# Performance work log

Measured on AMD Instinct MI355X. Metric: run time of the kernel, lower is better.

The kernel has to match this reference:

```python
import jax, jax.numpy as jnp
import numpy as np

NEG_SLOPE = 0.2  # PyG GATConv default negative_slope


def setup_inputs() -> dict:
    key = jax.random.key(0)
    ks = jax.random.split(key, 10)
    N, E, IN, H, C = 50000, 800000, 256, 4, 128
    return {
        "x": jax.random.normal(ks[0], (N, IN), jnp.float32),
        "edge_index": jax.random.randint(ks[1], (2, E), 0, N, jnp.int64),
        "W": jax.random.normal(ks[2], (IN, H * C), jnp.float32) * (1.0 / np.sqrt(IN)),
        "att_src": jax.random.normal(ks[3], (H, C), jnp.float32) * 0.1,
        "att_dst": jax.random.normal(ks[4], (H, C), jnp.float32) * 0.1,
        "gat_bias": jax.random.normal(ks[5], (C,), jnp.float32) * 0.01,
        "w1": jax.random.normal(ks[6], (C, C), jnp.float32) * (1.0 / np.sqrt(C)),
        "b1": jax.random.normal(ks[7], (C,), jnp.float32) * 0.01,
        "w2": jax.random.normal(ks[8], (C, 1), jnp.float32) * (1.0 / np.sqrt(C)),
        "b2": jax.random.normal(ks[9], (1,), jnp.float32) * 0.01,
    }


def _gat_conv(x, edge_index, W, att_src, att_dst, gat_bias):
    # PyG GATConv with concat=False (mean over heads), add_self_loops=True,
    # dropout inactive (eval mode).
    N = x.shape[0]
    H, C = att_src.shape
    xl = (x @ W).reshape(N, H, C)                       # [N,H,C] projected nodes
    a_src = jnp.einsum("nhc,hc->nh", xl, att_src)       # [N,H]
    a_dst = jnp.einsum("nhc,hc->nh", xl, att_dst)       # [N,H]
    loops = jnp.arange(N, dtype=edge_index.dtype)
    src = jnp.concatenate([edge_index[0], loops])        # [E+N]
    dst = jnp.concatenate([edge_index[1], loops])        # [E+N]
    logits = jax.nn.leaky_relu(a_src[src] + a_dst[dst], NEG_SLOPE)  # [E+N,H]
    # segment softmax over incoming edges of each dst node
    m = jax.ops.segment_max(logits, dst, num_segments=N)            # [N,H]
    e = jnp.exp(logits - m[dst])
    denom = jax.ops.segment_sum(e, dst, num_segments=N)             # [N,H]
    alpha = e / denom[dst]                                           # [E+N,H]
    # weighted scatter-add aggregation
    out = jax.ops.segment_sum(alpha[:, :, None] * xl[src], dst, num_segments=N)  # [N,H,C]
    return out.mean(axis=1) + gat_bias                   # concat=False -> head mean


def reference(x, edge_index, W, att_src, att_dst, gat_bias, w1, b1, w2, b2):
    h = _gat_conv(x, edge_index, W, att_src, att_dst, gat_bias)
    h = jax.nn.relu(h)
    h = jax.nn.relu(h @ w1 + b1)
    return (h @ w2 + b2)[:, 0]
```

## Files before the change

### kernel.cpp

```cpp
#include <hip/hip_runtime.h>
#include <hip/hip_bf16.h>


#define LEAKY(x) ((x) > 0.0f ? (x) : 0.2f * (x))
#define CAP 64

typedef __attribute__((ext_vector_type(8))) short short8v;
typedef __attribute__((ext_vector_type(4))) float floatx4;
typedef __attribute__((ext_vector_type(2))) float f32x2;
typedef __attribute__((ext_vector_type(2))) unsigned int u32x2;

__device__ __forceinline__ unsigned f2b(float f) {
    unsigned u = __float_as_uint(f);
    return (u + 0x7fffu + ((u >> 16) & 1u)) >> 16;
}

__device__ __forceinline__ float rlf(float v, int i) {
    return __uint_as_float(
        __builtin_amdgcn_readlane(__float_as_uint(v), (unsigned)i));
}

__device__ __forceinline__ void load_lds16(const void* g, void* lds) {
    __builtin_amdgcn_global_load_lds(
        (const __attribute__((address_space(1))) void*)g,
        (__attribute__((address_space(3))) void*)lds, 16, 0, 0);
}

__global__ __launch_bounds__(256) void prep_small(
    const float* __restrict__ W, const float* __restrict__ att_src,
    const float* __restrict__ att_dst, const float* __restrict__ w1,
    int* __restrict__ cnt, float* __restrict__ watt,
    ushort* __restrict__ WT2, ushort* __restrict__ w1t, int N) {
    int pb = blockIdx.x;
    int t = threadIdx.x;
    if (pb < 196) {
        int i = pb * 256 + t;
        if (i < N) cnt[i] = 0;
    } else if (pb < 204) {
        int idx = (pb - 196) * 256 + t;
        int k = idx >> 3;
        int h8 = idx & 7;
        int h = h8 & 3;
        const float* att = (h8 < 4) ? att_src : att_dst;
        const float* wrow = W + (size_t)k * 512 + h * 128;
        const float* arow = att + h * 128;
        float s = 0.f;
#pragma unroll 4
        for (int c = 0; c < 128; ++c) s += wrow[c] * arow[c];
        watt[h8 * 256 + k] = s;
    } else if (pb < 716) {
        int idx = (pb - 204) * 256 + t;
        int c = idx & 127;
        int h = (idx >> 7) & 3;
        int k = idx >> 9;
        WT2[c * 1024 + h * 256 + k] = (ushort)f2b(W[(size_t)k * 512 + h * 128 + c]);
    } else {
        int idx = (pb - 716) * 256 + t;
        int c = idx & 127;
        int k = idx >> 7;
        w1t[c * 128 + k] = (ushort)f2b(w1[(size_t)k * 128 + c]);
    }
}

__global__ void fill_lite(const int* __restrict__ ei, int E, int N,
                          int* __restrict__ cnt, int* __restrict__ esrc) {
    int e = blockIdx.x * 256 + threadIdx.x;
    if (e >= E + N) return;
    int s, d;
    if (e < E) {
        s = ei[e];
        d = ei[E + e];
    } else {
        s = d = e - E;
    }
    if (d < 0 || d >= N || s < 0 || s >= N) return;
    int slot = atomicAdd(&cnt[d], 1);
    if (slot < CAP) esrc[d * CAP + slot] = s;
}

__global__ __launch_bounds__(256) void cast_score(
    const float* __restrict__ x, const float* __restrict__ watt,
    ushort* __restrict__ xb, float* __restrict__ asrc,
    float* __restrict__ adst, int N) {
    int w = threadIdx.x >> 6, l = threadIdx.x & 63;
    int n = blockIdx.x * 4 + w;
    if (n >= N) return;
    float4 xv = *(const float4*)(x + (size_t)n * 256 + l * 4);
    ushort4 ub;
    ub.x = (ushort)f2b(xv.x);
    ub.y = (ushort)f2b(xv.y);
    ub.z = (ushort)f2b(xv.z);
    ub.w = (ushort)f2b(xv.w);
    *(ushort4*)(xb + (size_t)n * 256 + l * 4) = ub;

    float acc[8];
#pragma unroll
    for (int h8 = 0; h8 < 8; ++h8) {
        float4 wv = *(const float4*)(watt + h8 * 256 + l * 4);
        acc[h8] = xv.x * wv.x + xv.y * wv.y + xv.z * wv.z + xv.w * wv.w;
    }
#pragma unroll
    for (int o = 32; o; o >>= 1)
#pragma unroll
        for (int h8 = 0; h8 < 8; ++h8) acc[h8] += __shfl_xor(acc[h8], o);
    if (l == 0) {
#pragma unroll
        for (int h = 0; h < 4; ++h) {
            asrc[n * 4 + h] = acc[h];
            adst[n * 4 + h] = acc[4 + h];
        }
    }
}

#define EDGE_PK(w0, w1, w2, w3, g)                                           \
    {                                                                        \
        f32x2 _e01 = {__uint_as_float((g).x << 16),                          \
                      __uint_as_float((g).x & 0xffff0000u)};                 \
        f32x2 _e23 = {__uint_as_float((g).y << 16),                          \
                      __uint_as_float((g).y & 0xffff0000u)};                 \
        f32x2 _w;                                                            \
        _w = (f32x2){(w0), (w0)};                                            \
        acc[0][0] += _w * _e01; acc[0][1] += _w * _e23;                      \
        _w = (f32x2){(w1), (w1)};                                            \
        acc[1][0] += _w * _e01; acc[1][1] += _w * _e23;                      \
        _w = (f32x2){(w2), (w2)};                                            \
        acc[2][0] += _w * _e01; acc[2][1] += _w * _e23;                      \
        _w = (f32x2){(w3), (w3)};                                            \
        acc[3][0] += _w * _e01; acc[3][1] += _w * _e23;                      \
    }

__global__ __launch_bounds__(256) void aggregate_x(
    const ushort* __restrict__ xb, const int* __restrict__ cnt,
    const int* __restrict__ esrc, const float* __restrict__ asrc,
    const float* __restrict__ adst, ushort* __restrict__ G, int N) {
    const int t = threadIdx.x;
    const int wv = t >> 6, l = t & 63;
    const int n = blockIdx.x * 4 + wv;
    if (n >= N) return;
    const int beg = n * CAP;
    const int deg = min(cnt[n], CAP);
    const uint loff = (uint)l * 4u;

    float4 ad = ((const float4*)adst)[n];
    int s_l = 0;
    float4 wl = {0.f, 0.f, 0.f, 0.f};
    if (l < deg) {
        s_l = esrc[beg + l];
        float4 as = ((const float4*)asrc)[s_l];
        wl.x = __expf(LEAKY(as.x + ad.x));
        wl.y = __expf(LEAKY(as.y + ad.y));
        wl.z = __expf(LEAKY(as.z + ad.z));
        wl.w = __expf(LEAKY(as.w + ad.w));
    }
    float dx = wl.x, dy = wl.y, dz = wl.z, dw = wl.w;
#pragma unroll
    for (int o = 32; o; o >>= 1) {
        dx += __shfl_xor(dx, o);
        dy += __shfl_xor(dy, o);
        dz += __shfl_xor(dz, o);
        dw += __shfl_xor(dw, o);
    }
    const float sc[4] = {0.25f / dx, 0.25f / dy, 0.25f / dz, 0.25f / dw};

    f32x2 acc[4][2];
#pragma unroll
    for (int h = 0; h < 4; ++h) {
        acc[h][0] = (f32x2){0.f, 0.f};
        acc[h][1] = (f32x2){0.f, 0.f};
    }

    int i = 0;
    const int deg8 = deg & ~7;
    for (; i < deg8; i += 8) {
        int ss[8];
#pragma unroll
        for (int j = 0; j < 8; ++j)
            ss[j] = __builtin_amdgcn_readlane(s_l, i + j);
        uint2 gg[8];
#pragma unroll
        for (int j = 0; j < 8; ++j)
            gg[j] = *(const uint2*)(xb + ((uint)ss[j] * 256u + loff));
#pragma unroll
        for (int j = 0; j < 8; ++j) {
            float w0 = rlf(wl.x, i + j), w1 = rlf(wl.y, i + j);
            float w2 = rlf(wl.z, i + j), w3 = rlf(wl.w, i + j);
            EDGE_PK(w0, w1, w2, w3, gg[j]);
        }
    }
    for (; i < deg; ++i) {
        int s0 = __builtin_amdgcn_readlane(s_l, i);
        uint2 g0 = *(const uint2*)(xb + ((uint)s0 * 256u + loff));
        float w00 = rlf(wl.x, i), w01 = rlf(wl.y, i);
        float w02 = rlf(wl.z, i), w03 = rlf(wl.w, i);
        EDGE_PK(w00, w01, w02, w03, g0);
    }

#pragma unroll
    for (int h = 0; h < 4; ++h) {
        u32x2 o;
        o.x = f2b(acc[h][0][0] * sc[h]) | (f2b(acc[h][0][1] * sc[h]) << 16);
        o.y = f2b(acc[h][1][0] * sc[h]) | (f2b(acc[h][1][1] * sc[h]) << 16);
        *(u32x2*)(G + (size_t)n * 1024 + h * 256 + l * 4) = o;
    }
}

__global__ __launch_bounds__(256) void tail_kernel(
    const ushort* __restrict__ Gb,
    const ushort* __restrict__ Wstk,
    const ushort* __restrict__ w1t,
    const float* __restrict__ gat_bias, const float* __restrict__ b1,
    const float* __restrict__ w2, const float* __restrict__ b2,
    float* __restrict__ out, int N) {
    __shared__ char smem[33 * 1024];
    char* AlsB = smem;
    char* BlsB = smem + 16 * 1024;
    char* ndh = smem;
    float* sums = (float*)(smem + 32 * 1024);

    const int t = threadIdx.x;
    const int w = t >> 6;
    const int l = t & 63;
    const int wr = w >> 1, wc = w & 1;
    const int row0 = blockIdx.x * 128;

    float gbr[4], b1r[4], w2r[4];
#pragma unroll
    for (int n = 0; n < 4; ++n) {
        int cg = wc * 64 + n * 16 + (l & 15);
        gbr[n] = gat_bias[cg];
        b1r[n] = b1[cg];
        w2r[n] = w2[cg];
    }

    floatx4 acc[4][4];
#pragma unroll
    for (int m = 0; m < 4; ++m)
#pragma unroll
        for (int n = 0; n < 4; ++n) acc[m][n] = {0.f, 0.f, 0.f, 0.f};

    const int lr = l >> 3;
    const int kbyt = ((l & 7) ^ lr) << 4;
    const char* Abase = (const char*)Gb;
    const char* Bbase = (const char*)Wstk;

    for (int ks = 0; ks < 16; ++ks) {
        const int k0b = ks * 128;
#pragma unroll
        for (int c = 0; c < 4; ++c) {
            int rowt = w * 32 + c * 8 + lr;
            int rA = row0 + rowt;
            if (rA >= N) rA = N - 1;
            load_lds16(Abase + (size_t)rA * 2048 + k0b + kbyt,
                       AlsB + (w * 4 + c) * 1024);
            load_lds16(Bbase + (size_t)rowt * 2048 + k0b + kbyt,
                       BlsB + (w * 4 + c) * 1024);
        }
        __syncthreads();

#pragma unroll
        for (int kk = 0; kk < 2; ++kk) {
            const int kb_g = kk * 64 + (l >> 4) * 16;
            const int swz = (l & 7) << 4;
            short8v a[4], b[4];
#pragma unroll
            for (int m = 0; m < 4; ++m) {
                int row = wr * 64 + m * 16 + (l & 15);
                a[m] = *(const short8v*)(AlsB + row * 128 + (kb_g ^ swz));
            }
#pragma unroll
            for (int n = 0; n < 4; ++n) {
                int row = wc * 64 + n * 16 + (l & 15);
                b[n] = *(const short8v*)(BlsB + row * 128 + (kb_g ^ swz));
            }
#pragma unroll
            for (int m = 0; m < 4; ++m)
#pragma unroll
                for (int n = 0; n < 4; ++n)
                    acc[m][n] = __builtin_amdgcn_mfma_f32_16x16x32_bf16(
                        a[m], b[n], acc[m][n], 0, 0, 0);
        }
        __syncthreads();
    }

#pragma unroll
    for (int m = 0; m < 4; ++m) {
#pragma unroll
        for (int reg = 0; reg < 4; ++reg) {
            int r = wr * 64 + m * 16 + ((l >> 4) << 2) + reg;
            int srow = (r & 7) << 4;
#pragma unroll
            for (int n = 0; n < 4; ++n) {
                int c = wc * 64 + n * 16 + (l & 15);
                float v = acc[m][n][reg] + gbr[n];
                v = v > 0.f ? v : 0.f;
                *(ushort*)(ndh + r * 256 + ((2 * c) ^ srow)) = (ushort)f2b(v);
            }
        }
    }
    __syncthreads();

    floatx4 acc2[4][4];
#pragma unroll
    for (int m = 0; m < 4; ++m)
#pragma unroll
        for (int n = 0; n < 4; ++n) acc2[m][n] = {0.f, 0.f, 0.f, 0.f};

    const char* w1base = (const char*)w1t;
#pragma unroll
    for (int kk = 0; kk < 4; ++kk) {
        const int kb = kk * 64 + (l >> 4) * 16;
        short8v a2[4], b2f[4];
#pragma unroll
        for (int m = 0; m < 4; ++m) {
            int r = wr * 64 + m * 16 + (l & 15);
            a2[m] = *(const short8v*)(ndh + r * 256 + (kb ^ ((r & 7) << 4)));
        }
#pragma unroll
        for (int n = 0; n < 4; ++n) {
            int r = wc * 64 + n * 16 + (l & 15);
            b2f[n] = *(const short8v*)(w1base + r * 256 + kb);
        }
#pragma unroll
        for (int m = 0; m < 4; ++m)
#pragma unroll
            for (int n = 0; n < 4; ++n)
                acc2[m][n] = __builtin_amdgcn_mfma_f32_16x16x32_bf16(
                    a2[m], b2f[n], acc2[m][n], 0, 0, 0);
    }

    float part[4][4];
#pragma unroll
    for (int m = 0; m < 4; ++m)
#pragma unroll
        for (int reg = 0; reg < 4; ++reg) {
            float s = 0.f;
#pragma unroll
            for (int n = 0; n < 4; ++n) {
                float y = acc2[m][n][reg] + b1r[n];
                y = y > 0.f ? y : 0.f;
                s += y * w2r[n];
            }
            part[m][reg] = s;
        }
#pragma unroll
    for (int o = 1; o < 16; o <<= 1)
#pragma unroll
        for (int m = 0; m < 4; ++m)
#pragma unroll
            for (int reg = 0; reg < 4; ++reg)
                part[m][reg] += __shfl_xor(part[m][reg], o);
    if ((l & 15) == 0) {
#pragma unroll
        for (int m = 0; m < 4; ++m)
#pragma unroll
            for (int reg = 0; reg < 4; ++reg) {
                int r = wr * 64 + m * 16 + ((l >> 4) << 2) + reg;
                sums[wc * 128 + r] = part[m][reg];
            }
    }
    __syncthreads();
    if (t < 128) {
        int rg = row0 + t;
        if (rg < N) out[rg] = sums[t] + sums[128 + t] + b2[0];
    }
}

extern "C" void kernel_launch(void* const* d_in, const int* in_sizes, int n_in,
                              void* d_out, int out_size, void* d_ws,
                              size_t ws_size, hipStream_t stream) {
    const float* x = (const float*)d_in[0];
    const int* ei = (const int*)d_in[1];
    const float* W = (const float*)d_in[2];
    const float* att_src = (const float*)d_in[3];
    const float* att_dst = (const float*)d_in[4];
    const float* gat_bias = (const float*)d_in[5];
    const float* w1 = (const float*)d_in[6];
    const float* b1 = (const float*)d_in[7];
    const float* w2 = (const float*)d_in[8];
    const float* b2 = (const float*)d_in[9];
    float* out = (float*)d_out;

    const int N = in_sizes[0] / 256;
    const int E = in_sizes[1] / 2;

    size_t o = 0;
    char* wsb = (char*)d_ws;
    auto alloc = [&](size_t nbytes) -> void* {
        void* p = wsb + o;
        o += (nbytes + 255) & ~(size_t)255;
        return p;
    };
    float* asrc = (float*)alloc((size_t)N * 4 * 4);
    float* adst = (float*)alloc((size_t)N * 4 * 4);
    int* cnt = (int*)alloc((size_t)N * 4);
    int* esrc = (int*)alloc((size_t)N * CAP * 4);
    ushort* xb = (ushort*)alloc((size_t)N * 256 * 2);
    ushort* G = (ushort*)alloc((size_t)N * 1024 * 2);
    ushort* WT2 = (ushort*)alloc((size_t)128 * 1024 * 2);
    ushort* w1t = (ushort*)alloc((size_t)128 * 128 * 2);
    float* watt = (float*)alloc((size_t)8 * 256 * 4);

    prep_small<<<780, 256, 0, stream>>>(W, att_src, att_dst, w1, cnt, watt,
                                        WT2, w1t, N);
    cast_score<<<(N + 3) / 4, 256, 0, stream>>>(x, watt, xb, asrc, adst, N);
    fill_lite<<<(E + N + 255) / 256, 256, 0, stream>>>(ei, E, N, cnt, esrc);
    aggregate_x<<<(N + 3) / 4, 256, 0, stream>>>(xb, cnt, esrc, asrc, adst, G,
                                                 N);
    tail_kernel<<<(N + 127) / 128, 256, 0, stream>>>(
        G, WT2, w1t, gat_bias, b1, w2, b2, out, N);
}
```

Measured before the change: 198.2 us.

## Split wave into half-waves gathering two edges per step with 16-byte loads

The aggregation kernel now has each half of a wavefront gather a different source row. Every lane loads 16 bytes (8 bf16 channels) instead of 8, so two edges are processed per step, and the two halves' partial sums are combined with a cross-half shuffle before the bf16 store. This halves the number of gather load instructions and loop iterations per edge, at the cost of twice the accumulator registers and an extra reduction. The fill kernel also handles two edges per thread with half the blocks, which reduces launch and thread overhead.

Result: slower. 280.2 us (+41.4%).

```diff
diff --git a/kernel.cpp b/kernel.cpp
--- a/kernel.cpp
+++ b/kernel.cpp
@@ -8,7 +8,6 @@
 typedef __attribute__((ext_vector_type(8))) short short8v;
 typedef __attribute__((ext_vector_type(4))) float floatx4;
 typedef __attribute__((ext_vector_type(2))) float f32x2;
-typedef __attribute__((ext_vector_type(2))) unsigned int u32x2;
 
 __device__ __forceinline__ unsigned f2b(float f) {
     unsigned u = __float_as_uint(f);
@@ -64,18 +63,22 @@
 
 __global__ void fill_lite(const int* __restrict__ ei, int E, int N,
                           int* __restrict__ cnt, int* __restrict__ esrc) {
-    int e = blockIdx.x * 256 + threadIdx.x;
-    if (e >= E + N) return;
-    int s, d;
-    if (e < E) {
-        s = ei[e];
-        d = ei[E + e];
-    } else {
-        s = d = e - E;
-    }
-    if (d < 0 || d >= N || s < 0 || s >= N) return;
-    int slot = atomicAdd(&cnt[d], 1);
-    if (slot < CAP) esrc[d * CAP + slot] = s;
+    int base = (blockIdx.x * 256 + threadIdx.x) * 2;
+#pragma unroll
+    for (int q = 0; q < 2; ++q) {
+        int e = base + q;
+        if (e >= E + N) return;
+        int s, d;
+        if (e < E) {
+            s = ei[e];
+            d = ei[E + e];
+        } else {
+            s = d = e - E;
+        }
+        if (d < 0 || d >= N || s < 0 || s >= N) continue;
+        int slot = atomicAdd(&cnt[d], 1);
+        if (slot < CAP) esrc[d * CAP + slot] = s;
+    }
 }
 
 __global__ __launch_bounds__(256) void cast_score(
@@ -112,21 +115,27 @@
     }
 }
 
-#define EDGE_PK(w0, w1, w2, w3, g)                                           \
+#define BL(u) __uint_as_float((u) << 16)
+#define BH(u) __uint_as_float((u) & 0xffff0000u)
+#define PAIR_FMA(w0, w1, w2, w3, g)                                          \
     {                                                                        \
-        f32x2 _e01 = {__uint_as_float((g).x << 16),                          \
-                      __uint_as_float((g).x & 0xffff0000u)};                 \
-        f32x2 _e23 = {__uint_as_float((g).y << 16),                          \
-                      __uint_as_float((g).y & 0xffff0000u)};                 \
-        f32x2 _w;                                                            \
-        _w = (f32x2){(w0), (w0)};                                            \
-        acc[0][0] += _w * _e01; acc[0][1] += _w * _e23;                      \
-        _w = (f32x2){(w1), (w1)};                                            \
-        acc[1][0] += _w * _e01; acc[1][1] += _w * _e23;                      \
-        _w = (f32x2){(w2), (w2)};                                            \
-        acc[2][0] += _w * _e01; acc[2][1] += _w * _e23;                      \
-        _w = (f32x2){(w3), (w3)};                                            \
-        acc[3][0] += _w * _e01; acc[3][1] += _w * _e23;                      \
+        f32x2 _e0 = {BL((g).x), BH((g).x)};                                  \
+        f32x2 _e1 = {BL((g).y), BH((g).y)};                                  \
+        f32x2 _e2 = {BL((g).z), BH((g).z)};                                  \
+        f32x2 _e3 = {BL((g).w), BH((g).w)};                                  \
+        f32x2 _W;                                                            \
+        _W = (f32x2){(w0), (w0)};                                            \
+        acc[0][0] += _W * _e0; acc[0][1] += _W * _e1;                        \
+        acc[0][2] += _W * _e2; acc[0][3] += _W * _e3;                        \
+        _W = (f32x2){(w1), (w1)};                                            \
+        acc[1][0] += _W * _e0; acc[1][1] += _W * _e1;                        \
+        acc[1][2] += _W * _e2; acc[1][3] += _W * _e3;                        \
+        _W = (f32x2){(w2), (w2)};                                            \
+        acc[2][0] += _W * _e0; acc[2][1] += _W * _e1;                        \
+        acc[2][2] += _W * _e2; acc[2][3] += _W * _e3;                        \
+        _W = (f32x2){(w3), (w3)};                                            \
+        acc[3][0] += _W * _e0; acc[3][1] += _W * _e1;                        \
+        acc[3][2] += _W * _e2; acc[3][3] += _W * _e3;                        \
     }
 
 __global__ __launch_bounds__(256) void aggregate_x(
@@ -139,7 +148,8 @@
     if (n >= N) return;
     const int beg = n * CAP;
     const int deg = min(cnt[n], CAP);
-    const uint loff = (uint)l * 4u;
+    const int hf = l >> 5;
+    const uint coff = (uint)(l & 31) * 8u;
 
     float4 ad = ((const float4*)adst)[n];
     int s_l = 0;
@@ -162,45 +172,70 @@
     }
     const float sc[4] = {0.25f / dx, 0.25f / dy, 0.25f / dz, 0.25f / dw};
 
-    f32x2 acc[4][2];
-#pragma unroll
-    for (int h = 0; h < 4; ++h) {
-        acc[h][0] = (f32x2){0.f, 0.f};
-        acc[h][1] = (f32x2){0.f, 0.f};
-    }
+    f32x2 acc[4][4];
+#pragma unroll
+    for (int h = 0; h < 4; ++h)
+#pragma unroll
+        for (int c = 0; c < 4; ++c) acc[h][c] = (f32x2){0.f, 0.f};
 
     int i = 0;
-    const int deg8 = deg & ~7;
-    for (; i < deg8; i += 8) {
-        int ss[8];
-#pragma unroll
-        for (int j = 0; j < 8; ++j)
-            ss[j] = __builtin_amdgcn_readlane(s_l, i + j);
-        uint2 gg[8];
-#pragma unroll
-        for (int j = 0; j < 8; ++j)
-            gg[j] = *(const uint2*)(xb + ((uint)ss[j] * 256u + loff));
-#pragma unroll
-        for (int j = 0; j < 8; ++j) {
-            float w0 = rlf(wl.x, i + j), w1 = rlf(wl.y, i + j);
-            float w2 = rlf(wl.z, i + j), w3 = rlf(wl.w, i + j);
-            EDGE_PK(w0, w1, w2, w3, gg[j]);
-        }
-    }
-    for (; i < deg; ++i) {
-        int s0 = __builtin_amdgcn_readlane(s_l, i);
-        uint2 g0 = *(const uint2*)(xb + ((uint)s0 * 256u + loff));
-        float w00 = rlf(wl.x, i), w01 = rlf(wl.y, i);
-        float w02 = rlf(wl.z, i), w03 = rlf(wl.w, i);
-        EDGE_PK(w00, w01, w02, w03, g0);
-    }
-
-#pragma unroll
-    for (int h = 0; h < 4; ++h) {
-        u32x2 o;
+    for (; i + 8 <= deg; i += 8) {
+        uint4 g[4];
+#pragma unroll
+        for (int p = 0; p < 4; ++p) {
+            int se = __builtin_amdgcn_readlane(s_l, i + 2 * p);
+            int so = __builtin_amdgcn_readlane(s_l, i + 2 * p + 1);
+            int su = hf ? so : se;
+            g[p] = *(const uint4*)(xb + ((uint)su * 256u + coff));
+        }
+#pragma unroll
+        for (int p = 0; p < 4; ++p) {
+            int ie = i + 2 * p, io = ie + 1;
+            float w0 = hf ? rlf(wl.x, io) : rlf(wl.x, ie);
+            float w1 = hf ? rlf(wl.y, io) : rlf(wl.y, ie);
+            float w2 = hf ? rlf(wl.z, io) : rlf(wl.z, ie);
+            float w3 = hf ? rlf(wl.w, io) : rlf(wl.w, ie);
+            PAIR_FMA(w0, w1, w2, w3, g[p]);
+        }
+    }
+    for (; i + 2 <= deg; i += 2) {
+        int se = __builtin_amdgcn_readlane(s_l, i);
+        int so = __builtin_amdgcn_readlane(s_l, i + 1);
+        int su = hf ? so : se;
+        uint4 g = *(const uint4*)(xb + ((uint)su * 256u + coff));
+        float w0 = hf ? rlf(wl.x, i + 1) : rlf(wl.x, i);
+        float w1 = hf ? rlf(wl.y, i + 1) : rlf(wl.y, i);
+        float w2 = hf ? rlf(wl.z, i + 1) : rlf(wl.z, i);
+        float w3 = hf ? rlf(wl.w, i + 1) : rlf(wl.w, i);
+        PAIR_FMA(w0, w1, w2, w3, g);
+    }
+    if (i < deg) {
+        int se = __builtin_amdgcn_readlane(s_l, i);
+        uint4 g = *(const uint4*)(xb + ((uint)se * 256u + coff));
+        float w0 = hf ? 0.f : rlf(wl.x, i);
+        float w1 = hf ? 0.f : rlf(wl.y, i);
+        float w2 = hf ? 0.f : rlf(wl.z, i);
+        float w3 = hf ? 0.f : rlf(wl.w, i);
+        PAIR_FMA(w0, w1, w2, w3, g);
+    }
+
+#pragma unroll
+    for (int h = 0; h < 4; ++h)
+#pragma unroll
+        for (int c = 0; c < 4; ++c) {
+            acc[h][c][0] += __shfl_xor(acc[h][c][0], 32);
+            acc[h][c][1] += __shfl_xor(acc[h][c][1], 32);
+        }
+
+#pragma unroll
+    for (int hh = 0; hh < 2; ++hh) {
+        int h = 2 * hf + hh;
+        uint4 o;
         o.x = f2b(acc[h][0][0] * sc[h]) | (f2b(acc[h][0][1] * sc[h]) << 16);
         o.y = f2b(acc[h][1][0] * sc[h]) | (f2b(acc[h][1][1] * sc[h]) << 16);
-        *(u32x2*)(G + (size_t)n * 1024 + h * 256 + l * 4) = o;
+        o.z = f2b(acc[h][2][0] * sc[h]) | (f2b(acc[h][2][1] * sc[h]) << 16);
+        o.w = f2b(acc[h][3][0] * sc[h]) | (f2b(acc[h][3][1] * sc[h]) << 16);
+        *(uint4*)(G + (size_t)n * 1024 + h * 256 + coff) = o;
     }
 }
 
@@ -403,7 +438,7 @@
     prep_small<<<780, 256, 0, stream>>>(W, att_src, att_dst, w1, cnt, watt,
                                         WT2, w1t, N);
     cast_score<<<(N + 3) / 4, 256, 0, stream>>>(x, watt, xb, asrc, adst, N);
-    fill_lite<<<(E + N + 255) / 256, 256, 0, stream>>>(ei, E, N, cnt, esrc);
+    fill_lite<<<(E + N + 511) / 512, 256, 0, stream>>>(ei, E, N, cnt, esrc);
     aggregate_x<<<(N + 3) / 4, 256, 0, stream>>>(xb, cnt, esrc, asrc, adst, G,
                                                  N);
     tail_kernel<<<(N + 127) / 128, 256, 0, stream>>>(
```
